# Optimization experiments

Measured on AMD Instinct MI355X. Metric: run time of the kernel, lower is better.

The kernel has to match this reference:

```python
import jax, jax.numpy as jnp
import numpy as np

EMBED = 256
HEADS = 8
HEAD_DIM = 32
MLP_DIM = 1024
NEG = -1e9  # large negative in place of -inf so fully-deselected rows don't NaN
LN_EPS = 1e-5


def _layernorm(x, g, b):
    m = jnp.mean(x, axis=-1, keepdims=True)
    v = jnp.mean(jnp.square(x - m), axis=-1, keepdims=True)
    return (x - m) / jnp.sqrt(v + LN_EPS) * g + b


def setup_inputs() -> dict:
    key = jax.random.key(0)
    ks = jax.random.split(key, 16)
    b, s, d = 64, 360, EMBED
    sc = 0.02
    return {
        "x": jax.random.normal(ks[0], (b, s, d), dtype=jnp.float32),
        "attention_mask": jnp.zeros((b, 1, 1, s), dtype=jnp.float32),
        # TokenRouter.weight_predictor: Linear(256, 1)
        "wp_w": jax.random.normal(ks[1], (1, d), dtype=jnp.float32) * sc,
        "wp_b": jnp.zeros((1,), dtype=jnp.float32),
        # TokenRouter.aux_predictor: Linear(256,128) -> SiLU -> Linear(128,2)
        "a1_w": jax.random.normal(ks[2], (d // 2, d), dtype=jnp.float32) * sc,
        "a1_b": jnp.zeros((d // 2,), dtype=jnp.float32),
        "a2_w": jax.random.normal(ks[3], (2, d // 2), dtype=jnp.float32) * sc,
        "a2_b": jnp.zeros((2,), dtype=jnp.float32),
        # transformer block (pre-LN GPT2-style)
        "ln1_g": jnp.ones((d,), dtype=jnp.float32),
        "ln1_b": jnp.zeros((d,), dtype=jnp.float32),
        "wqkv": jax.random.normal(ks[4], (d, 3 * d), dtype=jnp.float32) * sc,
        "bqkv": jnp.zeros((3 * d,), dtype=jnp.float32),
        "wo": jax.random.normal(ks[5], (d, d), dtype=jnp.float32) * sc,
        "bo": jnp.zeros((d,), dtype=jnp.float32),
        "ln2_g": jnp.ones((d,), dtype=jnp.float32),
        "ln2_b": jnp.zeros((d,), dtype=jnp.float32),
        "w1": jax.random.normal(ks[6], (d, MLP_DIM), dtype=jnp.float32) * sc,
        "b1": jnp.zeros((MLP_DIM,), dtype=jnp.float32),
        "w2": jax.random.normal(ks[7], (MLP_DIM, d), dtype=jnp.float32) * sc,
        "b2": jnp.zeros((d,), dtype=jnp.float32),
    }


def reference(x, attention_mask, wp_w, wp_b, a1_w, a1_b, a2_w, a2_b,
              ln1_g, ln1_b, wqkv, bqkv, wo, bo, ln2_g, ln2_b, w1, b1, w2, b2):
    b, s, d = x.shape
    # --- router: per-token scalar weight ---
    weights = (x @ wp_w.T + wp_b).squeeze(-1)  # [b, s]
    # --- aux predictor selects tokens (eval path: argmax over 2 logits) ---
    h = jax.nn.silu(x @ a1_w.T + a1_b)
    aux_logits = h @ a2_w.T + a2_b            # [b, s, 2]
    sel = jnp.argmax(aux_logits, axis=-1).astype(bool)  # [b, s]
    # --- masked transformer block over the selected token subset.
    # Compacting tokens then attending == full-seq attention with deselected
    # keys masked out (LN/MLP/residual are position-wise), so vectorize:
    bias = attention_mask + jnp.where(sel, 0.0, NEG)[:, None, None, :]  # [b,1,1,s]
    hn = _layernorm(x, ln1_g, ln1_b)
    qkv = hn @ wqkv + bqkv
    q, k, v = jnp.split(qkv, 3, axis=-1)
    q = q.reshape(b, s, HEADS, HEAD_DIM)
    k = k.reshape(b, s, HEADS, HEAD_DIM)
    v = v.reshape(b, s, HEADS, HEAD_DIM)
    scores = jnp.einsum("bqhd,bkhd->bhqk", q, k) / np.sqrt(HEAD_DIM).astype(np.float32)
    scores = scores + bias                   # [b, h, s, s]
    attn = jax.nn.softmax(scores, axis=-1)
    ctx = jnp.einsum("bhqk,bkhd->bqhd", attn, v).reshape(b, s, d)
    h1 = x + (ctx @ wo + bo)
    h2n = _layernorm(h1, ln2_g, ln2_b)
    block_out = h1 + (jax.nn.gelu(h2n @ w1 + b1) @ w2 + b2)  # [b, s, d]
    # --- scatter-recombine: selected -> weighted block output, else passthrough
    out = jnp.where(sel[..., None], block_out * weights[..., None], x)
    avg_selected = jnp.sum(sel.astype(x.dtype)) / b
    return out, avg_selected
```

## Files before the change

kernel.cpp:

```cpp
#include <hip/hip_runtime.h>
#include <math.h>
#include <stdint.h>

#define TOKN 23040
#define BSZ 64
#define SEQ 360
#define DIM 256
#define NHD 8
#define HDD 32
#define MLPD 1024
#define NEGV -1e9f

typedef __attribute__((ext_vector_type(8))) short bf16x8;
typedef __attribute__((ext_vector_type(4))) float f32x4;

static __device__ __forceinline__ short f2bs(float f) {
  unsigned u = __builtin_bit_cast(unsigned, f);
  u += 0x7fffu + ((u >> 16) & 1u);
  return (short)(u >> 16);
}
static __device__ __forceinline__ float bf2f(short s) {
  unsigned u = ((unsigned)(unsigned short)s) << 16;
  return __builtin_bit_cast(float, u);
}
static __device__ __forceinline__ unsigned packbf(float a, float b) {
  return (unsigned)(unsigned short)f2bs(a) | ((unsigned)(unsigned short)f2bs(b) << 16);
}
static __device__ __forceinline__ void gl16(const short* g, short* l) {
  __builtin_amdgcn_global_load_lds(
      (const __attribute__((address_space(1))) unsigned int*)g,
      (__attribute__((address_space(3))) unsigned int*)l, 16, 0, 0);
}

__global__ __launch_bounds__(256) void convw_k(
    const float* __restrict__ wqkv, const float* __restrict__ wo,
    const float* __restrict__ w1, const float* __restrict__ w2,
    short* __restrict__ wqkvt, short* __restrict__ wot,
    short* __restrict__ w1t, short* __restrict__ w2t) {
  int id = blockIdx.x * 256 + threadIdx.x;
  if (id < 256 * 768) {
    int k = id / 768, n = id % 768;
    wqkvt[n * 256 + k] = f2bs(wqkv[id]);
  }
  if (id < 256 * 256) {
    int k = id >> 8, n = id & 255;
    wot[n * 256 + k] = f2bs(wo[id]);
  }
  if (id < 256 * 1024) {
    int k = id >> 10, n = id & 1023;
    w1t[n * 256 + k] = f2bs(w1[id]);
  }
  if (id < 1024 * 256) {
    int k = id >> 8, n = id & 255;
    w2t[n * 1024 + k] = f2bs(w2[id]);
  }
}

__global__ __launch_bounds__(256) void ln_router_k(
    const float* __restrict__ in, const float* __restrict__ g,
    const float* __restrict__ b, const float* __restrict__ wpw,
    const float* __restrict__ wpb, short* __restrict__ outn,
    float* __restrict__ wout, float* __restrict__ outx) {
  int tok = blockIdx.x * 4 + (threadIdx.x >> 6);
  int lane = threadIdx.x & 63;
  const float4 xv = *(const float4*)(in + (size_t)tok * DIM + lane * 4);
  *(float4*)(outx + (size_t)tok * DIM + lane * 4) = xv;
  float s = xv.x + xv.y + xv.z + xv.w;
  float s2 = xv.x * xv.x + xv.y * xv.y + xv.z * xv.z + xv.w * xv.w;
#pragma unroll
  for (int o = 1; o < 64; o <<= 1) { s += __shfl_xor(s, o); s2 += __shfl_xor(s2, o); }
  float m = s * (1.f / DIM);
  float var = fmaxf(s2 * (1.f / DIM) - m * m, 0.f);
  float rstd = rsqrtf(var + 1e-5f);
  float4 gv = *(const float4*)(g + lane * 4);
  float4 bv = *(const float4*)(b + lane * 4);
  uint2 pk;
  pk.x = packbf((xv.x - m) * rstd * gv.x + bv.x, (xv.y - m) * rstd * gv.y + bv.y);
  pk.y = packbf((xv.z - m) * rstd * gv.z + bv.z, (xv.w - m) * rstd * gv.w + bv.w);
  *(uint2*)(outn + (size_t)tok * DIM + lane * 4) = pk;
  float4 wv = *(const float4*)(wpw + lane * 4);
  float wd = xv.x * wv.x + xv.y * wv.y + xv.z * wv.z + xv.w * wv.w;
#pragma unroll
  for (int o = 1; o < 64; o <<= 1) wd += __shfl_xor(wd, o);
  if (lane == 0) wout[tok] = wd + wpb[0];
}

__global__ __launch_bounds__(256) void ln_k(
    const short* __restrict__ in, const float* __restrict__ g,
    const float* __restrict__ b, const int* __restrict__ mtotp,
    short* __restrict__ outn) {
  int tok = blockIdx.x * 4 + (threadIdx.x >> 6);
  int lane = threadIdx.x & 63;
  if (tok >= *mtotp) return;
  union { uint2 v; short s[4]; } u;
  u.v = *(const uint2*)(in + (size_t)tok * DIM + lane * 4);
  float x0 = bf2f(u.s[0]), x1 = bf2f(u.s[1]), x2 = bf2f(u.s[2]), x3 = bf2f(u.s[3]);
  float s = x0 + x1 + x2 + x3;
  float s2 = x0 * x0 + x1 * x1 + x2 * x2 + x3 * x3;
#pragma unroll
  for (int o = 1; o < 64; o <<= 1) { s += __shfl_xor(s, o); s2 += __shfl_xor(s2, o); }
  float m = s * (1.f / DIM);
  float var = fmaxf(s2 * (1.f / DIM) - m * m, 0.f);
  float rstd = rsqrtf(var + 1e-5f);
  float4 gv = *(const float4*)(g + lane * 4);
  float4 bv = *(const float4*)(b + lane * 4);
  uint2 pk;
  pk.x = packbf((x0 - m) * rstd * gv.x + bv.x, (x1 - m) * rstd * gv.y + bv.y);
  pk.y = packbf((x2 - m) * rstd * gv.z + bv.z, (x3 - m) * rstd * gv.w + bv.w);
  *(uint2*)(outn + (size_t)tok * DIM + lane * 4) = pk;
}

__global__ __launch_bounds__(256) void router_gemm_k(
    const float* __restrict__ x, const float* __restrict__ a1w,
    const float* __restrict__ a1b, const float* __restrict__ a2w,
    const float* __restrict__ a2b, int* __restrict__ sel) {
  __shared__ __align__(16) float XT[32][36];
  __shared__ __align__(16) float WT[32][128];
  int m0 = blockIdx.x * 32;
  int t = threadIdx.x;
  int tx = t & 31, ty = t >> 5;
  float acc[4][4] = {};
  int r = t >> 3, c = (t & 7) * 4;
  int n2 = t >> 1, c2 = (t & 1) * 16;
  for (int k0 = 0; k0 < 256; k0 += 32) {
    float4 xa = *(const float4*)(x + (size_t)(m0 + r) * 256 + k0 + c);
    XT[c + 0][r] = xa.x; XT[c + 1][r] = xa.y; XT[c + 2][r] = xa.z; XT[c + 3][r] = xa.w;
#pragma unroll
    for (int j = 0; j < 4; j++) {
      float4 wv = *(const float4*)(a1w + (size_t)n2 * 256 + k0 + c2 + j * 4);
      WT[c2 + j * 4 + 0][n2] = wv.x;
      WT[c2 + j * 4 + 1][n2] = wv.y;
      WT[c2 + j * 4 + 2][n2] = wv.z;
      WT[c2 + j * 4 + 3][n2] = wv.w;
    }
    __syncthreads();
#pragma unroll 8
    for (int kk = 0; kk < 32; kk++) {
      float4 wv4 = *(const float4*)&WT[kk][tx * 4];
      float4 xv4 = *(const float4*)&XT[kk][ty * 4];
      float xr[4] = {xv4.x, xv4.y, xv4.z, xv4.w};
      float wr[4] = {wv4.x, wv4.y, wv4.z, wv4.w};
#pragma unroll
      for (int i = 0; i < 4; i++)
#pragma unroll
        for (int j = 0; j < 4; j++) acc[i][j] += xr[i] * wr[j];
    }
    __syncthreads();
  }
  float b1v[4], a20[4], a21[4];
#pragma unroll
  for (int j = 0; j < 4; j++) {
    int dim = tx * 4 + j;
    b1v[j] = a1b[dim];
    a20[j] = a2w[dim];
    a21[j] = a2w[128 + dim];
  }
  float bias0 = a2b[0], bias1 = a2b[1];
#pragma unroll
  for (int i = 0; i < 4; i++) {
    float l0 = 0.f, l1 = 0.f;
#pragma unroll
    for (int j = 0; j < 4; j++) {
      float v = acc[i][j] + b1v[j];
      float h = v / (1.f + expf(-v));
      l0 += h * a20[j];
      l1 += h * a21[j];
    }
#pragma unroll
    for (int o = 1; o < 32; o <<= 1) { l0 += __shfl_xor(l0, o); l1 += __shfl_xor(l1, o); }
    if (tx == 0) sel[m0 + ty * 4 + i] = (l1 + bias1 > l0 + bias0) ? 1 : 0;
  }
}

__global__ __launch_bounds__(512) void scanA_k(const int* __restrict__ sel,
                                               int* __restrict__ idxl,
                                               int* __restrict__ cnt) {
  __shared__ int sc[512];
  int b = blockIdx.x, t = threadIdx.x;
  int flag = (t < SEQ) ? sel[b * SEQ + t] : 0;
  sc[t] = flag;
  __syncthreads();
  int val = flag;
  for (int off = 1; off < 512; off <<= 1) {
    int add = (t >= off) ? sc[t - off] : 0;
    __syncthreads();
    val += add;
    sc[t] = val;
    __syncthreads();
  }
  if (flag) idxl[b * SEQ + (val - 1)] = t;
  if (t == 511) cnt[b] = val;
}

__global__ __launch_bounds__(512) void scanB_k(const int* __restrict__ cnt,
                                               int* __restrict__ startp,
                                               int* __restrict__ mtotp,
                                               int* __restrict__ g_idx,
                                               float* __restrict__ outavg) {
  __shared__ int sc[64];
  __shared__ int mt;
  int t = threadIdx.x;
  if (t < 64) sc[t] = cnt[t];
  __syncthreads();
  if (t == 0) {
    int run = 0;
    for (int b = 0; b < 64; b++) { startp[b] = run; run += sc[b]; }
    *mtotp = run;
    mt = run;
    outavg[0] = (float)run / 64.0f;
  }
  __syncthreads();
  int m = mt;
  for (int i = m + t; i < TOKN; i += 512) g_idx[i] = 0;
}

__global__ __launch_bounds__(512) void scanC_k(const int* __restrict__ idxl,
                                               const int* __restrict__ startp,
                                               const int* __restrict__ cnt,
                                               int* __restrict__ g_idx) {
  int b = blockIdx.x, t = threadIdx.x;
  int c = cnt[b], s0 = startp[b];
  for (int j = t; j < c; j += 512) g_idx[s0 + j] = b * SEQ + idxl[b * SEQ + j];
}

template <int MODE>
__global__ __launch_bounds__(256) void gemm_bt_k(
    const short* __restrict__ A, const short* __restrict__ Bt,
    const float* __restrict__ bias, const float* __restrict__ resf,
    const short* __restrict__ resb, const float* __restrict__ wgt,
    const int* __restrict__ g_idx, const int* __restrict__ mtotp,
    short* __restrict__ outb, float* __restrict__ outf, int Ndim, int Kdim) {
  int Mt = *mtotp;
  int m0 = blockIdx.y * 64;
  if (m0 >= Mt) return;
  __shared__ __align__(16) short As0[64 * 32];
  __shared__ __align__(16) short As1[64 * 32];
  __shared__ __align__(16) short Bs0[64 * 32];
  __shared__ __align__(16) short Bs1[64 * 32];
  int n0 = blockIdx.x * 64;
  int t = threadIdx.x;
  int wave = t >> 6, lane = t & 63;
  int l15 = lane & 15, quad = lane >> 4;
  int wr = (wave >> 1) * 32, wc = (wave & 1) * 32;
  int r0 = t >> 2, c0 = (t & 3) * 8;
  long ar0 = (MODE == 0) ? g_idx[m0 + r0] : (m0 + r0);
  const short* gA = A + ar0 * Kdim + c0;
  const short* gB = Bt + (size_t)(n0 + r0) * Kdim + c0;
  short* lA0 = As0 + wave * 512;
  short* lA1 = As1 + wave * 512;
  short* lB0 = Bs0 + wave * 512;
  short* lB1 = Bs1 + wave * 512;

  f32x4 acc[2][2];
#pragma unroll
  for (int i = 0; i < 2; i++)
#pragma unroll
    for (int j = 0; j < 2; j++)
#pragma unroll
      for (int r = 0; r < 4; r++) acc[i][j][r] = 0.f;

  for (int k0 = 0; k0 < Kdim; k0 += 64) {
    gl16(gA + k0, lA0);
    gl16(gA + k0 + 32, lA1);
    gl16(gB + k0, lB0);
    gl16(gB + k0 + 32, lB1);
    __syncthreads();
    bf16x8 a0[2], a1[2], b0[2], b1[2];
#pragma unroll
    for (int i = 0; i < 2; i++) {
      a0[i] = *(const bf16x8*)&As0[(wr + i * 16 + l15) * 32 + quad * 8];
      a1[i] = *(const bf16x8*)&As1[(wr + i * 16 + l15) * 32 + quad * 8];
      b0[i] = *(const bf16x8*)&Bs0[(wc + i * 16 + l15) * 32 + quad * 8];
      b1[i] = *(const bf16x8*)&Bs1[(wc + i * 16 + l15) * 32 + quad * 8];
    }
#pragma unroll
    for (int i = 0; i < 2; i++)
#pragma unroll
      for (int j = 0; j < 2; j++) {
        acc[i][j] = __builtin_amdgcn_mfma_f32_16x16x32_bf16(a0[i], b0[j],
                                                            acc[i][j], 0, 0, 0);
        acc[i][j] = __builtin_amdgcn_mfma_f32_16x16x32_bf16(a1[i], b1[j],
                                                            acc[i][j], 0, 0, 0);
      }
    __syncthreads();
  }

#pragma unroll
  for (int i = 0; i < 2; i++) {
#pragma unroll
    for (int j = 0; j < 2; j++) {
      int col = n0 + wc + j * 16 + l15;
      float bcol = bias[col];
#pragma unroll
      for (int r = 0; r < 4; r++) {
        int row = m0 + wr + i * 16 + quad * 4 + r;
        float v = acc[i][j][r] + bcol;
        size_t idx = (size_t)row * Ndim + col;
        if (MODE == 0) {
          outb[idx] = f2bs(v);
        } else if (MODE == 1) {
          int orig = g_idx[row];
          outb[idx] = f2bs(v + resf[(size_t)orig * 256 + col]);
        } else if (MODE == 2) {
          float u = 0.7978845608028654f * (v + 0.044715f * v * v * v);
          float e = __expf(2.f * u);
          float th = 1.f - 2.f / (e + 1.f);
          outb[idx] = f2bs(0.5f * v * (1.f + th));
        } else {
          if (row < Mt) {
            int orig = g_idx[row];
            float o = (v + bf2f(resb[idx])) * wgt[orig];
            outf[(size_t)orig * 256 + col] = o;
          }
        }
      }
    }
  }
}

__global__ __launch_bounds__(256) void attn_k(
    const short* __restrict__ qkv, const float* __restrict__ amask,
    const int* __restrict__ g_idx, const int* __restrict__ startp,
    const int* __restrict__ cntp, short* __restrict__ ctx) {
  __shared__ __align__(16) short VF[2 * 12 * 64 * 8];
  __shared__ __align__(16) float ls[384];
  int bh = blockIdx.x >> 1, qhalf = blockIdx.x & 1;
  int bb = bh >> 3, h = bh & 7;
  int t = threadIdx.x;
  int start = startp[bb], cnt = cntp[bb];
  size_t base = (size_t)start * 768;
  for (int i = t; i < 1536; i += 256) {
    int k = i >> 2, cg = (i & 3) * 8;
    union { int4 v; short s[8]; } u;
    if (k < cnt) {
      u.v = *(const int4*)(qkv + base + (size_t)k * 768 + 512 + h * 32 + cg);
    } else {
      u.v = make_int4(0, 0, 0, 0);
    }
    int c = k >> 5, qd = (k >> 3) & 3, j = k & 7;
#pragma unroll
    for (int jj = 0; jj < 8; jj++) {
      int d = cg + jj;
      VF[((((d >> 4) * 12 + c) * 64) + qd * 16 + (d & 15)) * 8 + j] = u.s[jj];
    }
  }
  for (int i = t; i < 384; i += 256)
    ls[i] = (i < cnt) ? amask[g_idx[start + i]] : 0.f;
  __syncthreads();

  int wave = t >> 6, lane = t & 63;
  int ql = lane & 15, quad = lane >> 4;
  int addr0 = (((quad & 1) * 2) * 16 + ql) * 4;
  int addr1 = addr0 + 64;
  bool hiq = quad >= 2;
  int nt = (cnt + 15) >> 4;
  int nc = (cnt + 31) >> 5;

  for (int qt = qhalf + 2 * wave; qt < nt; qt += 8) {
    int q0 = qt * 16, qrow = q0 + ql;
    bf16x8 qf;
#pragma unroll
    for (int j = 0; j < 8; j++) qf[j] = 0;
    if (qrow < cnt)
      qf = *(const bf16x8*)(qkv + base + (size_t)qrow * 768 + h * 32 + quad * 8);

    f32x4 o0, o1;
#pragma unroll
    for (int r = 0; r < 4; r++) { o0[r] = 0.f; o1[r] = 0.f; }
    float lsum = 0.f;

    for (int c = 0; c < nc; c++) {
      int keyA = c * 32 + ql;
      int keyB = keyA + 16;
      bf16x8 kfA, kfB;
#pragma unroll
      for (int j = 0; j < 8; j++) { kfA[j] = 0; kfB[j] = 0; }
      if (keyA < cnt)
        kfA = *(const bf16x8*)(qkv + base + (size_t)keyA * 768 + 256 + h * 32 + quad * 8);
      if (keyB < cnt)
        kfB = *(const bf16x8*)(qkv + base + (size_t)keyB * 768 + 256 + h * 32 + quad * 8);
      f32x4 sa, sb;
#pragma unroll
      for (int r = 0; r < 4; r++) { sa[r] = 0.f; sb[r] = 0.f; }
      sa = __builtin_amdgcn_mfma_f32_16x16x32_bf16(kfA, qf, sa, 0, 0, 0);
      sb = __builtin_amdgcn_mfma_f32_16x16x32_bf16(kfB, qf, sb, 0, 0, 0);
      int kbase = c * 32 + quad * 4;
      float4 la = *(const float4*)&ls[kbase];
      float4 lb = *(const float4*)&ls[kbase + 16];
      float ea0 = (kbase + 0 < cnt) ? __expf(sa[0] * 0.17677669529663687f + la.x) : 0.f;
      float ea1 = (kbase + 1 < cnt) ? __expf(sa[1] * 0.17677669529663687f + la.y) : 0.f;
      float ea2 = (kbase + 2 < cnt) ? __expf(sa[2] * 0.17677669529663687f + la.z) : 0.f;
      float ea3 = (kbase + 3 < cnt) ? __expf(sa[3] * 0.17677669529663687f + la.w) : 0.f;
      float eb0 = (kbase + 16 < cnt) ? __expf(sb[0] * 0.17677669529663687f + lb.x) : 0.f;
      float eb1 = (kbase + 17 < cnt) ? __expf(sb[1] * 0.17677669529663687f + lb.y) : 0.f;
      float eb2 = (kbase + 18 < cnt) ? __expf(sb[2] * 0.17677669529663687f + lb.z) : 0.f;
      float eb3 = (kbase + 19 < cnt) ? __expf(sb[3] * 0.17677669529663687f + lb.w) : 0.f;
      lsum += (ea0 + ea1) + (ea2 + ea3) + (eb0 + eb1) + (eb2 + eb3);
      unsigned pA0 = packbf(ea0, ea1), pA1 = packbf(ea2, ea3);
      unsigned pB0 = packbf(eb0, eb1), pB1 = packbf(eb2, eb3);
      int s00 = __builtin_amdgcn_ds_bpermute(addr0, (int)pA0);
      int s10 = __builtin_amdgcn_ds_bpermute(addr0, (int)pB0);
      int s01 = __builtin_amdgcn_ds_bpermute(addr0, (int)pA1);
      int s11 = __builtin_amdgcn_ds_bpermute(addr0, (int)pB1);
      int s02 = __builtin_amdgcn_ds_bpermute(addr1, (int)pA0);
      int s12 = __builtin_amdgcn_ds_bpermute(addr1, (int)pB0);
      int s03 = __builtin_amdgcn_ds_bpermute(addr1, (int)pA1);
      int s13 = __builtin_amdgcn_ds_bpermute(addr1, (int)pB1);
      union { int i[4]; bf16x8 v; } pf;
      pf.i[0] = hiq ? s10 : s00;
      pf.i[1] = hiq ? s11 : s01;
      pf.i[2] = hiq ? s12 : s02;
      pf.i[3] = hiq ? s13 : s03;
      bf16x8 v0 = *(const bf16x8*)&VF[(c * 64 + lane) * 8];
      bf16x8 v1 = *(const bf16x8*)&VF[((12 + c) * 64 + lane) * 8];
      o0 = __builtin_amdgcn_mfma_f32_16x16x32_bf16(v0, pf.v, o0, 0, 0, 0);
      o1 = __builtin_amdgcn_mfma_f32_16x16x32_bf16(v1, pf.v, o1, 0, 0, 0);
    }
    lsum += __shfl_xor(lsum, 16);
    lsum += __shfl_xor(lsum, 32);
    float inv = 1.f / lsum;

    if (qrow < cnt) {
      size_t cb = ((size_t)(start + qrow)) * 256 + h * 32;
      uint2 w0, w1;
      w0.x = packbf(o0[0] * inv, o0[1] * inv);
      w0.y = packbf(o0[2] * inv, o0[3] * inv);
      w1.x = packbf(o1[0] * inv, o1[1] * inv);
      w1.y = packbf(o1[2] * inv, o1[3] * inv);
      *(uint2*)(ctx + cb + quad * 4) = w0;
      *(uint2*)(ctx + cb + 16 + quad * 4) = w1;
    }
  }
}

extern "C" void kernel_launch(void* const* d_in, const int* in_sizes, int n_in,
                              void* d_out, int out_size, void* d_ws,
                              size_t ws_size, hipStream_t stream) {
  const float* x = (const float*)d_in[0];
  const float* amask = (const float*)d_in[1];
  const float* wp_w = (const float*)d_in[2];
  const float* wp_b = (const float*)d_in[3];
  const float* a1_w = (const float*)d_in[4];
  const float* a1_b = (const float*)d_in[5];
  const float* a2_w = (const float*)d_in[6];
  const float* a2_b = (const float*)d_in[7];
  const float* ln1_g = (const float*)d_in[8];
  const float* ln1_b = (const float*)d_in[9];
  const float* wqkv = (const float*)d_in[10];
  const float* bqkv = (const float*)d_in[11];
  const float* wo = (const float*)d_in[12];
  const float* bo = (const float*)d_in[13];
  const float* ln2_g = (const float*)d_in[14];
  const float* ln2_b = (const float*)d_in[15];
  const float* w1 = (const float*)d_in[16];
  const float* b1 = (const float*)d_in[17];
  const float* w2 = (const float*)d_in[18];
  const float* b2 = (const float*)d_in[19];
  float* out = (float*)d_out;

  uint8_t* p = (uint8_t*)d_ws;
  float* weightsv = (float*)p; p += (size_t)TOKN * 4;
  int* selv = (int*)p;         p += (size_t)TOKN * 4;
  int* idxlv = (int*)p;        p += (size_t)TOKN * 4;
  int* gidxv = (int*)p;        p += (size_t)TOKN * 4;
  int* cntv = (int*)p;         p += 64 * 4;
  int* startv = (int*)p;       p += 64 * 4;
  int* mtotv = (int*)p;        p += 64 * 4;
  short* wqkvt = (short*)p;    p += (size_t)768 * 256 * 2;
  short* wot = (short*)p;      p += (size_t)256 * 256 * 2;
  short* w1t = (short*)p;      p += (size_t)1024 * 256 * 2;
  short* w2t = (short*)p;      p += (size_t)256 * 1024 * 2;
  short* h1bv = (short*)p;     p += (size_t)TOKN * 256 * 2;
  short* h2nv = (short*)p;     p += (size_t)TOKN * 256 * 2;
  short* ctxv = (short*)p;     p += (size_t)TOKN * 256 * 2;
  uint8_t* R = p;
  short* xnv = (short*)R;
  short* qkvv = (short*)(R + (size_t)TOKN * 256 * 2);
  short* actv = (short*)R;

  convw_k<<<dim3(1024), dim3(256), 0, stream>>>(wqkv, wo, w1, w2, wqkvt, wot, w1t, w2t);
  ln_router_k<<<dim3(TOKN / 4), dim3(256), 0, stream>>>(x, ln1_g, ln1_b, wp_w, wp_b,
                                                        xnv, weightsv, out);
  router_gemm_k<<<dim3(720), dim3(256), 0, stream>>>(x, a1_w, a1_b, a2_w, a2_b, selv);
  scanA_k<<<dim3(64), dim3(512), 0, stream>>>(selv, idxlv, cntv);
  scanB_k<<<dim3(1), dim3(512), 0, stream>>>(cntv, startv, mtotv, gidxv,
                                             out + (size_t)TOKN * 256);
  scanC_k<<<dim3(64), dim3(512), 0, stream>>>(idxlv, startv, cntv, gidxv);
  gemm_bt_k<0><<<dim3(12, 360), dim3(256), 0, stream>>>(
      xnv, wqkvt, bqkv, nullptr, nullptr, nullptr, gidxv, mtotv, qkvv, nullptr,
      768, 256);
  attn_k<<<dim3(1024), dim3(256), 0, stream>>>(qkvv, amask, gidxv, startv, cntv, ctxv);
  gemm_bt_k<1><<<dim3(4, 360), dim3(256), 0, stream>>>(
      ctxv, wot, bo, x, nullptr, nullptr, gidxv, mtotv, h1bv, nullptr, 256, 256);
  ln_k<<<dim3(TOKN / 4), dim3(256), 0, stream>>>(h1bv, ln2_g, ln2_b, mtotv, h2nv);
  gemm_bt_k<2><<<dim3(16, 360), dim3(256), 0, stream>>>(
      h2nv, w1t, b1, nullptr, nullptr, nullptr, gidxv, mtotv, actv, nullptr,
      1024, 256);
  gemm_bt_k<3><<<dim3(4, 360), dim3(256), 0, stream>>>(
      actv, w2t, b2, nullptr, h1bv, weightsv, gidxv, mtotv, nullptr, out, 256, 1024);
}
```

Measured before the change: 248.6 us.

## Use 128-row MFMA GEMM tiles and tiled weight transpose; trim index zeroing

Adds a gemm128_k kernel with 128xBN tiles, where each wave computes a 64-row strip over a double 32-wide K sub-block per iteration. It replaces the 64-row GEMMs for the QKV, MLP-up and MLP-down projections to raise data reuse per block and cut the number of blocks. The weight conversion kernel now transposes through a padded shared-memory tile so both its reads and writes are coalesced. scanB zeroes only the padding tail of the gather index instead of the whole remainder. Larger tiles mean more registers per thread and more wasted rows in the final partial tile.

Result: no change. 250.7 us (+0.9%).

```diff
diff --git a/kernel.cpp b/kernel.cpp
--- a/kernel.cpp
+++ b/kernel.cpp
@@ -37,23 +37,33 @@
     const float* __restrict__ w1, const float* __restrict__ w2,
     short* __restrict__ wqkvt, short* __restrict__ wot,
     short* __restrict__ w1t, short* __restrict__ w2t) {
-  int id = blockIdx.x * 256 + threadIdx.x;
-  if (id < 256 * 768) {
-    int k = id / 768, n = id % 768;
-    wqkvt[n * 256 + k] = f2bs(wqkv[id]);
-  }
-  if (id < 256 * 256) {
-    int k = id >> 8, n = id & 255;
-    wot[n * 256 + k] = f2bs(wo[id]);
-  }
-  if (id < 256 * 1024) {
-    int k = id >> 10, n = id & 1023;
-    w1t[n * 256 + k] = f2bs(w1[id]);
-  }
-  if (id < 1024 * 256) {
-    int k = id >> 8, n = id & 255;
-    w2t[n * 1024 + k] = f2bs(w2[id]);
-  }
+  __shared__ float tile[32][33];
+  int bid = blockIdx.x;
+  const float* src;
+  short* dst;
+  int K, N, kt, nt;
+  if (bid < 192) {
+    src = wqkv; dst = wqkvt; K = 256; N = 768; kt = bid / 24; nt = bid % 24;
+  } else if (bid < 256) {
+    int b = bid - 192; src = wo; dst = wot; K = 256; N = 256; kt = b >> 3; nt = b & 7;
+  } else if (bid < 512) {
+    int b = bid - 256; src = w1; dst = w1t; K = 256; N = 1024; kt = b >> 5; nt = b & 31;
+  } else {
+    int b = bid - 512; src = w2; dst = w2t; K = 1024; N = 256; kt = b >> 3; nt = b & 7;
+  }
+  int t = threadIdx.x, r = t >> 3, c4 = (t & 7) * 4;
+  const float4 v = *(const float4*)(src + (size_t)(kt * 32 + r) * N + nt * 32 + c4);
+  tile[c4 + 0][r] = v.x;
+  tile[c4 + 1][r] = v.y;
+  tile[c4 + 2][r] = v.z;
+  tile[c4 + 3][r] = v.w;
+  __syncthreads();
+  union { short s[4]; uint2 u; } o;
+  o.s[0] = f2bs(tile[r][c4 + 0]);
+  o.s[1] = f2bs(tile[r][c4 + 1]);
+  o.s[2] = f2bs(tile[r][c4 + 2]);
+  o.s[3] = f2bs(tile[r][c4 + 3]);
+  *(uint2*)(dst + (size_t)(nt * 32 + r) * K + kt * 32 + c4) = o.u;
 }
 
 __global__ __launch_bounds__(256) void ln_router_k(
@@ -211,7 +221,9 @@
   }
   __syncthreads();
   int m = mt;
-  for (int i = m + t; i < TOKN; i += 512) g_idx[i] = 0;
+  int e = m + 256;
+  if (e > TOKN) e = TOKN;
+  for (int i = m + t; i < e; i += 512) g_idx[i] = 0;
 }
 
 __global__ __launch_bounds__(512) void scanC_k(const int* __restrict__ idxl,
@@ -301,6 +313,116 @@
         } else if (MODE == 1) {
           int orig = g_idx[row];
           outb[idx] = f2bs(v + resf[(size_t)orig * 256 + col]);
+        } else if (MODE == 2) {
+          float u = 0.7978845608028654f * (v + 0.044715f * v * v * v);
+          float e = __expf(2.f * u);
+          float th = 1.f - 2.f / (e + 1.f);
+          outb[idx] = f2bs(0.5f * v * (1.f + th));
+        } else {
+          if (row < Mt) {
+            int orig = g_idx[row];
+            float o = (v + bf2f(resb[idx])) * wgt[orig];
+            outf[(size_t)orig * 256 + col] = o;
+          }
+        }
+      }
+    }
+  }
+}
+
+template <int MODE, int BN>
+__global__ __launch_bounds__(256) void gemm128_k(
+    const short* __restrict__ A, const short* __restrict__ Bt,
+    const float* __restrict__ bias, const float* __restrict__ resf,
+    const short* __restrict__ resb, const float* __restrict__ wgt,
+    const int* __restrict__ g_idx, const int* __restrict__ mtotp,
+    short* __restrict__ outb, float* __restrict__ outf, int Ndim, int Kdim) {
+  int Mt = *mtotp;
+  int m0 = blockIdx.y * 128;
+  if (m0 >= Mt) return;
+  __shared__ __align__(16) short As0[128 * 32];
+  __shared__ __align__(16) short As1[128 * 32];
+  __shared__ __align__(16) short Bs0[BN * 32];
+  __shared__ __align__(16) short Bs1[BN * 32];
+  constexpr int NJ = BN / 32;
+  int n0 = blockIdx.x * BN;
+  int t = threadIdx.x;
+  int wave = t >> 6, lane = t & 63;
+  int l15 = lane & 15, quad = lane >> 4;
+  int wr = (wave >> 1) * 64, wc = (wave & 1) * (BN / 2);
+  int r0 = t >> 2, c0 = (t & 3) * 8;
+  long arA = (MODE == 0) ? g_idx[m0 + r0] : (m0 + r0);
+  long arB = (MODE == 0) ? g_idx[m0 + 64 + r0] : (m0 + 64 + r0);
+  const short* gA0 = A + arA * Kdim + c0;
+  const short* gA1 = A + arB * Kdim + c0;
+  const short* gB0 = Bt + (size_t)(n0 + r0) * Kdim + c0;
+  const short* gB1 = Bt + (size_t)(n0 + 64 + r0) * Kdim + c0;
+  short* lA0 = As0 + wave * 512;
+  short* lA1 = As1 + wave * 512;
+  short* lB0 = Bs0 + wave * 512;
+  short* lB1 = Bs1 + wave * 512;
+
+  f32x4 acc[4][NJ];
+#pragma unroll
+  for (int i = 0; i < 4; i++)
+#pragma unroll
+    for (int j = 0; j < NJ; j++)
+#pragma unroll
+      for (int r = 0; r < 4; r++) acc[i][j][r] = 0.f;
+
+  for (int k0 = 0; k0 < Kdim; k0 += 64) {
+    gl16(gA0 + k0, lA0);
+    gl16(gA1 + k0, lA0 + 2048);
+    gl16(gA0 + k0 + 32, lA1);
+    gl16(gA1 + k0 + 32, lA1 + 2048);
+    gl16(gB0 + k0, lB0);
+    gl16(gB0 + k0 + 32, lB1);
+    if constexpr (BN == 128) {
+      gl16(gB1 + k0, lB0 + 2048);
+      gl16(gB1 + k0 + 32, lB1 + 2048);
+    }
+    __syncthreads();
+    bf16x8 af[4], bfr[NJ];
+#pragma unroll
+    for (int i = 0; i < 4; i++)
+      af[i] = *(const bf16x8*)&As0[(wr + i * 16 + l15) * 32 + quad * 8];
+#pragma unroll
+    for (int j = 0; j < NJ; j++)
+      bfr[j] = *(const bf16x8*)&Bs0[(wc + j * 16 + l15) * 32 + quad * 8];
+#pragma unroll
+    for (int i = 0; i < 4; i++)
+#pragma unroll
+      for (int j = 0; j < NJ; j++)
+        acc[i][j] = __builtin_amdgcn_mfma_f32_16x16x32_bf16(af[i], bfr[j],
+                                                            acc[i][j], 0, 0, 0);
+#pragma unroll
+    for (int i = 0; i < 4; i++)
+      af[i] = *(const bf16x8*)&As1[(wr + i * 16 + l15) * 32 + quad * 8];
+#pragma unroll
+    for (int j = 0; j < NJ; j++)
+      bfr[j] = *(const bf16x8*)&Bs1[(wc + j * 16 + l15) * 32 + quad * 8];
+#pragma unroll
+    for (int i = 0; i < 4; i++)
+#pragma unroll
+      for (int j = 0; j < NJ; j++)
+        acc[i][j] = __builtin_amdgcn_mfma_f32_16x16x32_bf16(af[i], bfr[j],
+                                                            acc[i][j], 0, 0, 0);
+    __syncthreads();
+  }
+
+#pragma unroll
+  for (int i = 0; i < 4; i++) {
+#pragma unroll
+    for (int j = 0; j < NJ; j++) {
+      int col = n0 + wc + j * 16 + l15;
+      float bcol = bias[col];
+#pragma unroll
+      for (int r = 0; r < 4; r++) {
+        int row = m0 + wr + i * 16 + quad * 4 + r;
+        float v = acc[i][j][r] + bcol;
+        size_t idx = (size_t)row * Ndim + col;
+        if (MODE == 0) {
+          outb[idx] = f2bs(v);
         } else if (MODE == 2) {
           float u = 0.7978845608028654f * (v + 0.044715f * v * v * v);
           float e = __expf(2.f * u);
@@ -478,7 +600,7 @@
   short* qkvv = (short*)(R + (size_t)TOKN * 256 * 2);
   short* actv = (short*)R;
 
-  convw_k<<<dim3(1024), dim3(256), 0, stream>>>(wqkv, wo, w1, w2, wqkvt, wot, w1t, w2t);
+  convw_k<<<dim3(768), dim3(256), 0, stream>>>(wqkv, wo, w1, w2, wqkvt, wot, w1t, w2t);
   ln_router_k<<<dim3(TOKN / 4), dim3(256), 0, stream>>>(x, ln1_g, ln1_b, wp_w, wp_b,
                                                         xnv, weightsv, out);
   router_gemm_k<<<dim3(720), dim3(256), 0, stream>>>(x, a1_w, a1_b, a2_w, a2_b, selv);
@@ -486,16 +608,16 @@
   scanB_k<<<dim3(1), dim3(512), 0, stream>>>(cntv, startv, mtotv, gidxv,
                                              out + (size_t)TOKN * 256);
   scanC_k<<<dim3(64), dim3(512), 0, stream>>>(idxlv, startv, cntv, gidxv);
-  gemm_bt_k<0><<<dim3(12, 360), dim3(256), 0, stream>>>(
+  gemm128_k<0, 128><<<dim3(6, 180), dim3(256), 0, stream>>>(
       xnv, wqkvt, bqkv, nullptr, nullptr, nullptr, gidxv, mtotv, qkvv, nullptr,
       768, 256);
   attn_k<<<dim3(1024), dim3(256), 0, stream>>>(qkvv, amask, gidxv, startv, cntv, ctxv);
   gemm_bt_k<1><<<dim3(4, 360), dim3(256), 0, stream>>>(
       ctxv, wot, bo, x, nullptr, nullptr, gidxv, mtotv, h1bv, nullptr, 256, 256);
   ln_k<<<dim3(TOKN / 4), dim3(256), 0, stream>>>(h1bv, ln2_g, ln2_b, mtotv, h2nv);
-  gemm_bt_k<2><<<dim3(16, 360), dim3(256), 0, stream>>>(
+  gemm128_k<2, 128><<<dim3(8, 180), dim3(256), 0, stream>>>(
       h2nv, w1t, b1, nullptr, nullptr, nullptr, gidxv, mtotv, actv, nullptr,
       1024, 256);
-  gemm_bt_k<3><<<dim3(4, 360), dim3(256), 0, stream>>>(
+  gemm128_k<3, 64><<<dim3(4, 180), dim3(256), 0, stream>>>(
       actv, w2t, b2, nullptr, h1bv, weightsv, gidxv, mtotv, nullptr, out, 256, 1024);
 }
```
